# Performance work log

Measured on AMD Instinct MI355X. Metric: run time of the kernel, lower is better.

Reference implementation:

```python
import jax, jax.numpy as jnp
import numpy as np


def _conv2d(x, w, b):
    # x: [B,C,H,W], w: [O,I,kh,kw] (SAME padding, stride 1)
    y = jax.lax.conv_general_dilated(x, w, (1, 1), 'SAME',
                                     dimension_numbers=('NCHW', 'OIHW', 'NCHW'))
    return y + b[None, :, None, None]


def _conv1x1(x, w, b):
    # w: [O,C], b: [O]
    return jnp.einsum('oc,bchw->bohw', w, x) + b[None, :, None, None]


def _attention(xq, xkv, w, b):
    # w: [3,C,C] (q,k,v), b: [3,C]. Tokens = spatial positions, features = channels.
    B, C, H, W = xq.shape
    q = _conv1x1(xq, w[0], b[0]).reshape(B, C, H * W).transpose(0, 2, 1)   # [B,HW,C]
    k = _conv1x1(xkv, w[1], b[1]).reshape(B, C, H * W).transpose(0, 2, 1)
    v = _conv1x1(xkv, w[2], b[2]).reshape(B, C, H * W).transpose(0, 2, 1)
    scale = 1.0 / jnp.sqrt(jnp.asarray(C, xq.dtype))  # d_k = channels
    a = jax.nn.softmax(jnp.einsum('bnc,bmc->bnm', q, k) * scale, axis=-1)  # [B,HW,HW]
    out = jnp.einsum('bnm,bmc->bnc', a, v).transpose(0, 2, 1).reshape(B, C, H, W)
    return out + xq


def _cell(x, h, c, w, b):
    gates = _conv2d(jnp.concatenate([x, h], axis=1), w, b)
    i, f, o, g = jnp.split(gates, 4, axis=1)
    i, f, o, g = jax.nn.sigmoid(i), jax.nn.sigmoid(f), jax.nn.sigmoid(o), jnp.tanh(g)
    c_new = f * c + i * g
    h_new = o * jnp.tanh(c_new)
    return h_new, c_new


def setup_inputs() -> dict:
    key = jax.random.key(0)
    ks = iter(jax.random.split(key, 32))
    B, T, Cin, H, W = 2, 3, 1, 32, 32
    HID, L, K, OUT = 64, 2, 3, 1
    s = 0.02
    d = {
        'x1_seq': jax.random.normal(next(ks), (B, T, Cin, H, W), jnp.float32),
        'x2_seq': jax.random.normal(next(ks), (B, T, Cin, H, W), jnp.float32),
        # ConvLSTM gate convs: layer0 in = Cin+HID, layer1 in = 2*HID, per stream
        'conv1_w0': jax.random.normal(next(ks), (4 * HID, Cin + HID, K, K)) * s,
        'conv1_b0': jnp.zeros((4 * HID,)),
        'conv1_w1': jax.random.normal(next(ks), (4 * HID, 2 * HID, K, K)) * s,
        'conv1_b1': jnp.zeros((4 * HID,)),
        'conv2_w0': jax.random.normal(next(ks), (4 * HID, Cin + HID, K, K)) * s,
        'conv2_b0': jnp.zeros((4 * HID,)),
        'conv2_w1': jax.random.normal(next(ks), (4 * HID, 2 * HID, K, K)) * s,
        'conv2_b1': jnp.zeros((4 * HID,)),
        # attention 1x1 convs, stacked [L, 3(q/k/v), HID, HID]
        'sah_w': jax.random.normal(next(ks), (L, 3, HID, HID)) * s,
        'sah_b': jnp.zeros((L, 3, HID)),
        'sac_w': jax.random.normal(next(ks), (L, 3, HID, HID)) * s,
        'sac_b': jnp.zeros((L, 3, HID)),
        'cah_w': jax.random.normal(next(ks), (L, 3, HID, HID)) * s,
        'cah_b': jnp.zeros((L, 3, HID)),
        'cac_w': jax.random.normal(next(ks), (L, 3, HID, HID)) * s,
        'cac_b': jnp.zeros((L, 3, HID)),
        # decoder
        'dec_w1': jax.random.normal(next(ks), (HID, HID, 3, 3)) * s,
        'dec_b1': jnp.zeros((HID,)),
        'dec_w2': jax.random.normal(next(ks), (OUT, HID, 3, 3)) * s,
        'dec_b2': jnp.zeros((OUT,)),
        'future_steps': 4,
    }
    return d


def reference(x1_seq, x2_seq,
              conv1_w0, conv1_b0, conv1_w1, conv1_b1,
              conv2_w0, conv2_b0, conv2_w1, conv2_b1,
              sah_w, sah_b, sac_w, sac_b, cah_w, cah_b, cac_w, cac_b,
              dec_w1, dec_b1, dec_w2, dec_b2, future_steps):
    B, T, _, H, W = x1_seq.shape
    HID = sah_w.shape[-1]
    L = sah_w.shape[0]
    cw1 = [(conv1_w0, conv1_b0), (conv1_w1, conv1_b1)]
    cw2 = [(conv2_w0, conv2_b0), (conv2_w1, conv2_b1)]

    def decoder(h):
        return _conv2d(jax.nn.relu(_conv2d(h, dec_w1, dec_b1)), dec_w2, dec_b2)

    z = jnp.zeros((B, HID, H, W), x1_seq.dtype)
    h1s, c1s = [z] * L, [z] * L
    h2s, c2s = [z] * L, [z] * L

    def step(x1_t, x2_t, h1s, c1s, h2s, c2s):
        h1s, c1s, h2s, c2s = list(h1s), list(c1s), list(h2s), list(c2s)
        for l in range(L):
            h1, c1 = _cell(x1_t, h1s[l], c1s[l], *cw1[l])
            h2, c2 = _cell(x2_t, h2s[l], c2s[l], *cw2[l])
            h1 = _attention(h1, h1, sah_w[l], sah_b[l])
            c1 = _attention(c1, c1, sac_w[l], sac_b[l])
            h2 = _attention(h2, h2, sah_w[l], sah_b[l])
            c2 = _attention(c2, c2, sac_w[l], sac_b[l])
            tag_h1, tag_c1 = h1, c1
            h1 = _attention(h1, h2, cah_w[l], cah_b[l])
            c1 = _attention(c1, c2, cac_w[l], cac_b[l])
            h2 = _attention(h2, tag_h1, cah_w[l], cah_b[l])
            c2 = _attention(c2, tag_c1, cac_w[l], cac_b[l])
            h1s[l], c1s[l], h2s[l], c2s[l] = h1, c1, h2, c2
            x1_t, x2_t = h1, h2
        return h1s, c1s, h2s, c2s

    warm1, warm2 = [], []
    for t in range(T):
        h1s, c1s, h2s, c2s = step(x1_seq[:, t], x2_seq[:, t], h1s, c1s, h2s, c2s)
        if t < T - 1:
            warm1.append(h1s[-1])
            warm2.append(h2s[-1])
    pred_warm1 = jnp.stack([decoder(h) for h in warm1], axis=1)
    pred_warm2 = jnp.stack([decoder(h) for h in warm2], axis=1)

    preds1, preds2 = [], []
    for _ in range(int(future_steps)):
        p1 = decoder(h1s[-1])
        p2 = decoder(h2s[-1])
        preds1.append(p1)
        preds2.append(p2)
        h1s, c1s, h2s, c2s = step(p1, p2, h1s, c1s, h2s, c2s)
    preds1 = jnp.stack(preds1, axis=1)
    preds2 = jnp.stack(preds2, axis=1)
    return preds1, preds2, pred_warm1, pred_warm2
```

## Files before the change

### kernel.cpp

```cpp
#include <hip/hip_runtime.h>
#include <math.h>

#define BB 2
#define HIDC 64
#define HWN 1024

struct TWArgs { const float* src[5]; float* dst[5]; int icn9[5]; int osh[5]; };

__global__ __launch_bounds__(256) void transpose_w(TWArgs a) {
  const int arr = blockIdx.y;
  const int icn9 = a.icn9[arr], osh = a.osh[arr];
  const int ocn = 1 << osh;
  const float* s = a.src[arr];
  float* d = a.dst[arr];
  const int n = icn9 << osh;
  for (int i = blockIdx.x * 256 + threadIdx.x; i < n; i += gridDim.x * 256) {
    int oc = i & (ocn - 1), tt = i >> osh;
    d[i] = s[(size_t)oc * icn9 + tt];
  }
}

struct CellArgs {
  const float* x[2]; long xbs;
  const float* h[2]; const float* c[2];
  const float* w[2]; const float* bias[2];
  float* ho[2]; float* co[2];
};

template<int CX>
__global__ __launch_bounds__(512) void cell_kernel(CellArgs a) {
  constexpr int CT = CX + HIDC;
  constexpr int CH = (CT + 1) / 2;
  __shared__ float sIn[CT * 48];
  __shared__ float sGa[256 * 17];
  __shared__ float sGb[256 * 17];
  const int tile = blockIdx.x;
  const int b = blockIdx.y;
  const int st = blockIdx.z;
  const int ty0 = (tile >> 3) << 2, tx0 = (tile & 7) << 2;
  const float* xp = a.x[st] + (size_t)b * a.xbs;
  const float* hp = a.h[st] + (size_t)b * HIDC * HWN;

  for (int idx = threadIdx.x; idx < CT * 36; idx += 512) {
    int ic = idx / 36, pos = idx - ic * 36;
    int iy = pos / 6, ix = pos - iy * 6;
    int gy = ty0 - 1 + iy, gx = tx0 - 1 + ix;
    float v = 0.f;
    if ((unsigned)gy < 32u && (unsigned)gx < 32u) {
      v = (ic < CX) ? xp[ic * HWN + gy * 32 + gx]
                    : hp[(ic - CX) * HWN + gy * 32 + gx];
    }
    sIn[ic * 48 + iy * 8 + ix] = v;
  }
  __syncthreads();

  const int oc = threadIdx.x & 255;
  const int hh = threadIdx.x >> 8;
  const int icb = hh ? CH : 0, ice = hh ? CT : CH;
  float acc[16];
#pragma unroll
  for (int p = 0; p < 16; ++p) acc[p] = 0.f;
  const float* wp = a.w[st];
  for (int ic = icb; ic < ice; ++ic) {
    float w9[9];
#pragma unroll
    for (int t = 0; t < 9; ++t) w9[t] = wp[(ic * 9 + t) * 256 + oc];
    float in[36];
#pragma unroll
    for (int iy = 0; iy < 6; ++iy) {
      float4 v4 = *(const float4*)&sIn[ic * 48 + iy * 8];
      float2 v2 = *(const float2*)&sIn[ic * 48 + iy * 8 + 4];
      in[iy * 6 + 0] = v4.x; in[iy * 6 + 1] = v4.y; in[iy * 6 + 2] = v4.z;
      in[iy * 6 + 3] = v4.w; in[iy * 6 + 4] = v2.x; in[iy * 6 + 5] = v2.y;
    }
#pragma unroll
    for (int ky = 0; ky < 3; ++ky)
#pragma unroll
      for (int kx = 0; kx < 3; ++kx) {
        const float wv = w9[ky * 3 + kx];
#pragma unroll
        for (int py = 0; py < 4; ++py)
#pragma unroll
          for (int px = 0; px < 4; ++px)
            acc[py * 4 + px] += wv * in[(py + ky) * 6 + (px + kx)];
      }
  }
  float* sGh = hh ? sGb : sGa;
#pragma unroll
  for (int p = 0; p < 16; ++p) sGh[oc * 17 + p] = acc[p];
  __syncthreads();

  const float* cp = a.c[st] + (size_t)b * HIDC * HWN;
  float* hop = a.ho[st] + (size_t)b * HIDC * HWN;
  float* cop = a.co[st] + (size_t)b * HIDC * HWN;
  const float* bias = a.bias[st];
  for (int idx = threadIdx.x; idx < HIDC * 16; idx += 512) {
    int hc = idx >> 4, p = idx & 15;
    float gi = sGa[hc * 17 + p]         + sGb[hc * 17 + p]         + bias[hc];
    float gf = sGa[(hc + 64) * 17 + p]  + sGb[(hc + 64) * 17 + p]  + bias[hc + 64];
    float go = sGa[(hc + 128) * 17 + p] + sGb[(hc + 128) * 17 + p] + bias[hc + 128];
    float gg = sGa[(hc + 192) * 17 + p] + sGb[(hc + 192) * 17 + p] + bias[hc + 192];
    gi = 1.f / (1.f + expf(-gi));
    gf = 1.f / (1.f + expf(-gf));
    go = 1.f / (1.f + expf(-go));
    gg = tanhf(gg);
    int off = hc * HWN + (ty0 + (p >> 2)) * 32 + tx0 + (p & 3);
    float cn = gf * cp[off] + gi * gg;
    cop[off] = cn;
    hop[off] = go * tanhf(cn);
  }
}

struct QkvArgs {
  const float* xq[4]; const float* xkv[4];
  const float* w[4]; const float* bias[4];
  float* Q; float* K; float* V;
};

__global__ __launch_bounds__(256) void qkv_kernel(QkvArgs a) {
  __shared__ float sWt[64 * 68];
  const int ptile = blockIdx.x, b = blockIdx.y;
  const int attn = blockIdx.z / 3, proj = blockIdx.z % 3;
  const float* x = (proj == 0 ? a.xq[attn] : a.xkv[attn]) + (size_t)b * HIDC * HWN;
  const float* w = a.w[attn] + proj * 64 * 64;
  const float* bias = a.bias[attn] + proj * 64;
  const size_t bb = (size_t)attn * BB + b;
  for (int i = threadIdx.x; i < 4096; i += 256) {
    int o = i >> 6, c = i & 63;
    sWt[c * 68 + o] = w[i];
  }
  __syncthreads();
  const int pq = threadIdx.x & 63, og = threadIdx.x >> 6;
  const int p0 = ptile * 64 + pq;
  float acc[16];
#pragma unroll
  for (int k = 0; k < 16; ++k) acc[k] = bias[og * 16 + k];
  for (int c = 0; c < 64; ++c) {
    float xv = x[c * HWN + p0];
#pragma unroll
    for (int k = 0; k < 16; k += 4) {
      float4 wv = *(const float4*)&sWt[c * 68 + og * 16 + k];
      acc[k+0] += xv * wv.x; acc[k+1] += xv * wv.y;
      acc[k+2] += xv * wv.z; acc[k+3] += xv * wv.w;
    }
  }
  if (proj == 1) {
    float* dK = a.K + bb * HIDC * HWN;
#pragma unroll
    for (int k = 0; k < 16; ++k)
      dK[(size_t)(og * 16 + k) * HWN + p0] = acc[k];
  } else {
    float* dst = (proj == 0 ? a.Q : a.V) + bb * HWN * HIDC;
    float* d = dst + (size_t)p0 * HIDC + og * 16;
#pragma unroll
    for (int k = 0; k < 16; k += 4) {
      float4 v; v.x = acc[k]; v.y = acc[k+1]; v.z = acc[k+2]; v.w = acc[k+3];
      *(float4*)&d[k] = v;
    }
  }
}

struct AttnPArgs { const float* Q; const float* Kt; const float* V; float* pbuf; };

__global__ __launch_bounds__(256) void attn_part(AttnPArgs a) {
  __shared__ float sQt[64 * 64];
  __shared__ float sPt[64 * 64];
  const int qt = blockIdx.x >> 3, ks = blockIdx.x & 7;
  const int b = blockIdx.y, at = blockIdx.z;
  const size_t bb = (size_t)at * BB + b;
  const float* Qp  = a.Q  + bb * HWN * HIDC + (size_t)qt * 64 * HIDC;
  const float* Ktp = a.Kt + bb * HIDC * HWN;
  const float* Vp  = a.V  + bb * HWN * HIDC;
  const int tid = threadIdx.x;
  {
    const int qr = tid & 63, qc0 = (tid >> 6) * 16;
    const float* q = Qp + qr * HIDC + qc0;
#pragma unroll
    for (int k = 0; k < 16; k += 4) {
      float4 v = *(const float4*)&q[k];
      sQt[(qc0 + k + 0) * 64 + qr] = v.x * 0.125f;
      sQt[(qc0 + k + 1) * 64 + qr] = v.y * 0.125f;
      sQt[(qc0 + k + 2) * 64 + qr] = v.z * 0.125f;
      sQt[(qc0 + k + 3) * 64 + qr] = v.w * 0.125f;
    }
  }
  const int tc = tid & 15, tr = tid >> 4;
  const int j0 = tc * 4, r0 = tr * 4;
  float m[4], l[4], o[4][4];
#pragma unroll
  for (int i = 0; i < 4; ++i) {
    m[i] = -1e30f; l[i] = 0.f;
    o[i][0] = 0; o[i][1] = 0; o[i][2] = 0; o[i][3] = 0;
  }
  __syncthreads();

  for (int kk = 0; kk < 2; ++kk) {
    const int jg = (ks * 2 + kk) * 64;
    float s[4][4];
#pragma unroll
    for (int i = 0; i < 4; ++i) { s[i][0]=0; s[i][1]=0; s[i][2]=0; s[i][3]=0; }
    const float* kp = Ktp + jg + j0;
#pragma unroll 8
    for (int c = 0; c < 64; ++c) {
      float4 q4 = *(const float4*)&sQt[c * 64 + r0];
      float4 k4 = *(const float4*)&kp[(size_t)c * HWN];
      s[0][0]+=q4.x*k4.x; s[0][1]+=q4.x*k4.y; s[0][2]+=q4.x*k4.z; s[0][3]+=q4.x*k4.w;
      s[1][0]+=q4.y*k4.x; s[1][1]+=q4.y*k4.y; s[1][2]+=q4.y*k4.z; s[1][3]+=q4.y*k4.w;
      s[2][0]+=q4.z*k4.x; s[2][1]+=q4.z*k4.y; s[2][2]+=q4.z*k4.z; s[2][3]+=q4.z*k4.w;
      s[3][0]+=q4.w*k4.x; s[3][1]+=q4.w*k4.y; s[3][2]+=q4.w*k4.z; s[3][3]+=q4.w*k4.w;
    }
    float mt[4];
#pragma unroll
    for (int i = 0; i < 4; ++i)
      mt[i] = fmaxf(fmaxf(s[i][0], s[i][1]), fmaxf(s[i][2], s[i][3]));
#pragma unroll
    for (int d = 1; d < 16; d <<= 1) {
#pragma unroll
      for (int i = 0; i < 4; ++i) mt[i] = fmaxf(mt[i], __shfl_xor(mt[i], d));
    }
    float al[4];
#pragma unroll
    for (int i = 0; i < 4; ++i) {
      float mn = fmaxf(m[i], mt[i]);
      al[i] = __expf(m[i] - mn);
      m[i] = mn;
      s[i][0] = __expf(s[i][0] - mn); s[i][1] = __expf(s[i][1] - mn);
      s[i][2] = __expf(s[i][2] - mn); s[i][3] = __expf(s[i][3] - mn);
    }
    float ps[4];
#pragma unroll
    for (int i = 0; i < 4; ++i) ps[i] = s[i][0] + s[i][1] + s[i][2] + s[i][3];
#pragma unroll
    for (int d = 1; d < 16; d <<= 1) {
#pragma unroll
      for (int i = 0; i < 4; ++i) ps[i] += __shfl_xor(ps[i], d);
    }
#pragma unroll
    for (int i = 0; i < 4; ++i) {
      l[i] = l[i] * al[i] + ps[i];
      o[i][0] *= al[i]; o[i][1] *= al[i]; o[i][2] *= al[i]; o[i][3] *= al[i];
    }
    __syncthreads();
#pragma unroll
    for (int jj = 0; jj < 4; ++jj) {
      int j = j0 + jj;
      float4 pv; pv.x = s[0][jj]; pv.y = s[1][jj]; pv.z = s[2][jj]; pv.w = s[3][jj];
      *(float4*)&sPt[j * 64 + (r0 ^ ((j & 7) * 4))] = pv;
    }
    __syncthreads();
    const float* vp = Vp + (size_t)jg * HIDC + j0;
#pragma unroll 8
    for (int j = 0; j < 64; ++j) {
      float4 p4 = *(const float4*)&sPt[j * 64 + (r0 ^ ((j & 7) * 4))];
      float4 v4 = *(const float4*)&vp[(size_t)j * HIDC];
      o[0][0]+=p4.x*v4.x; o[0][1]+=p4.x*v4.y; o[0][2]+=p4.x*v4.z; o[0][3]+=p4.x*v4.w;
      o[1][0]+=p4.y*v4.x; o[1][1]+=p4.y*v4.y; o[1][2]+=p4.y*v4.z; o[1][3]+=p4.y*v4.w;
      o[2][0]+=p4.z*v4.x; o[2][1]+=p4.z*v4.y; o[2][2]+=p4.z*v4.z; o[2][3]+=p4.z*v4.w;
      o[3][0]+=p4.w*v4.x; o[3][1]+=p4.w*v4.y; o[3][2]+=p4.w*v4.z; o[3][3]+=p4.w*v4.w;
    }
  }
  float* pb = a.pbuf + ((bb * 16 + qt) * 8 + ks) * 4224;
#pragma unroll
  for (int i = 0; i < 4; ++i) {
    float4 w; w.x = o[i][0]; w.y = o[i][1]; w.z = o[i][2]; w.w = o[i][3];
    *(float4*)&pb[(r0 + i) * 64 + j0] = w;
  }
  if (tc == 0) {
#pragma unroll
    for (int i = 0; i < 4; ++i) {
      pb[4096 + r0 + i] = m[i];
      pb[4160 + r0 + i] = l[i];
    }
  }
}

struct AttnMArgs { const float* pbuf; const float* xq[4]; float* out[4]; };

__global__ __launch_bounds__(256) void attn_merge(AttnMArgs a) {
  __shared__ float sW[8][64];
  __shared__ float sL[64];
  const int qt = blockIdx.x, b = blockIdx.y, at = blockIdx.z;
  const float* pb = a.pbuf + (((size_t)at * BB + b) * 16 + qt) * 8 * 4224;
  if (threadIdx.x < 64) {
    int r = threadIdx.x;
    float mm[8];
#pragma unroll
    for (int i = 0; i < 8; ++i) mm[i] = pb[i * 4224 + 4096 + r];
    float M = mm[0];
#pragma unroll
    for (int i = 1; i < 8; ++i) M = fmaxf(M, mm[i]);
    float L = 0.f;
#pragma unroll
    for (int i = 0; i < 8; ++i) {
      float w = __expf(mm[i] - M);
      sW[i][r] = w;
      L += pb[i * 4224 + 4160 + r] * w;
    }
    sL[r] = L;
  }
  __syncthreads();
  const int c = threadIdx.x >> 2, rg = (threadIdx.x & 3) * 16;
  const float* xq = a.xq[at] + (size_t)b * HIDC * HWN;
  float* op = a.out[at] + (size_t)b * HIDC * HWN;
  const int p0 = qt * 64 + rg;
#pragma unroll
  for (int rr4 = 0; rr4 < 16; rr4 += 4) {
    float rv[4];
#pragma unroll
    for (int k = 0; k < 4; ++k) {
      int r = rg + rr4 + k;
      float acc = 0.f;
#pragma unroll
      for (int i = 0; i < 8; ++i) acc += pb[i * 4224 + r * 64 + c] * sW[i][r];
      rv[k] = acc / sL[r];
    }
    float4 x4 = *(const float4*)&xq[(size_t)c * HWN + p0 + rr4];
    float4 res; res.x = rv[0] + x4.x; res.y = rv[1] + x4.y;
    res.z = rv[2] + x4.z; res.w = rv[3] + x4.w;
    *(float4*)&op[(size_t)c * HWN + p0 + rr4] = res;
  }
}

struct Dec1Args { const float* in[2]; const float* w; const float* b; float* tmp; };

__global__ __launch_bounds__(512) void dec1_kernel(Dec1Args a) {
  __shared__ float sIn[64 * 48];
  __shared__ float sHa[64 * 17];
  __shared__ float sHb[64 * 17];
  const int tile = blockIdx.x, b = blockIdx.y, st = blockIdx.z;
  const int ty0 = (tile >> 3) << 2, tx0 = (tile & 7) << 2;
  const float* ip = a.in[st] + (size_t)b * HIDC * HWN;
  for (int idx = threadIdx.x; idx < 64 * 36; idx += 512) {
    int ic = idx / 36, pos = idx - ic * 36;
    int iy = pos / 6, ix = pos - iy * 6;
    int gy = ty0 - 1 + iy, gx = tx0 - 1 + ix;
    float v = 0.f;
    if ((unsigned)gy < 32u && (unsigned)gx < 32u) v = ip[ic * HWN + gy * 32 + gx];
    sIn[ic * 48 + iy * 8 + ix] = v;
  }
  __syncthreads();
  const int oc = threadIdx.x & 63, ps = (threadIdx.x >> 6) & 3;
  const int hh = threadIdx.x >> 8;
  const int icb = hh * 32, ice = icb + 32;
  float acc0 = 0.f, acc1 = 0.f, acc2 = 0.f, acc3 = 0.f;
  const float* wp = a.w;
  for (int ic = icb; ic < ice; ++ic) {
    float w9[9];
#pragma unroll
    for (int t = 0; t < 9; ++t) w9[t] = wp[(ic * 9 + t) * 64 + oc];
    float in[18];
#pragma unroll
    for (int ry = 0; ry < 3; ++ry) {
      float4 v4 = *(const float4*)&sIn[ic * 48 + (ps + ry) * 8];
      float2 v2 = *(const float2*)&sIn[ic * 48 + (ps + ry) * 8 + 4];
      in[ry*6+0]=v4.x; in[ry*6+1]=v4.y; in[ry*6+2]=v4.z; in[ry*6+3]=v4.w;
      in[ry*6+4]=v2.x; in[ry*6+5]=v2.y;
    }
#pragma unroll
    for (int ky = 0; ky < 3; ++ky)
#pragma unroll
      for (int kx = 0; kx < 3; ++kx) {
        float wv = w9[ky * 3 + kx];
        acc0 += wv * in[ky * 6 + kx + 0];
        acc1 += wv * in[ky * 6 + kx + 1];
        acc2 += wv * in[ky * 6 + kx + 2];
        acc3 += wv * in[ky * 6 + kx + 3];
      }
  }
  float* sH = hh ? sHb : sHa;
  sH[oc * 17 + ps * 4 + 0] = acc0;
  sH[oc * 17 + ps * 4 + 1] = acc1;
  sH[oc * 17 + ps * 4 + 2] = acc2;
  sH[oc * 17 + ps * 4 + 3] = acc3;
  __syncthreads();
  float* dst = a.tmp + ((size_t)st * BB + b) * HIDC * HWN;
  for (int idx = threadIdx.x; idx < 1024; idx += 512) {
    int oc2 = idx >> 4, p = idx & 15;
    float v = sHa[oc2 * 17 + p] + sHb[oc2 * 17 + p] + a.b[oc2];
    v = fmaxf(v, 0.f);
    dst[(size_t)oc2 * HWN + (ty0 + (p >> 2)) * 32 + tx0 + (p & 3)] = v;
  }
}

struct Dec2Args { const float* tmp; const float* w; const float* b;
                  float* dst0; float* dst1; long bstr; };

__global__ __launch_bounds__(256) void dec2_kernel(Dec2Args a) {
  __shared__ float sIn[64 * 48];
  __shared__ float sW[64 * 9];
  const int tile = blockIdx.x, b = blockIdx.y, st = blockIdx.z;
  const int ty0 = (tile >> 3) << 2, tx0 = (tile & 7) << 2;
  const float* ip = a.tmp + ((size_t)st * BB + b) * HIDC * HWN;
  for (int idx = threadIdx.x; idx < 64 * 36; idx += 256) {
    int ic = idx / 36, pos = idx - ic * 36;
    int iy = pos / 6, ix = pos - iy * 6;
    int gy = ty0 - 1 + iy, gx = tx0 - 1 + ix;
    float v = 0.f;
    if ((unsigned)gy < 32u && (unsigned)gx < 32u) v = ip[ic * HWN + gy * 32 + gx];
    sIn[ic * 48 + iy * 8 + ix] = v;
  }
  for (int idx = threadIdx.x; idx < 576; idx += 256) sW[idx] = a.w[idx];
  __syncthreads();
  const int px = threadIdx.x >> 4, icg = threadIdx.x & 15;
  const int py = px >> 2, pxx = px & 3;
  float acc = 0.f;
#pragma unroll
  for (int i = 0; i < 4; ++i) {
    int ic = icg * 4 + i;
    const float* row = &sIn[ic * 48];
    const float* wv = &sW[ic * 9];
#pragma unroll
    for (int ky = 0; ky < 3; ++ky)
#pragma unroll
      for (int kx = 0; kx < 3; ++kx)
        acc += wv[ky * 3 + kx] * row[(py + ky) * 8 + pxx + kx];
  }
#pragma unroll
  for (int d = 1; d < 16; d <<= 1) acc += __shfl_xor(acc, d);
  if (icg == 0) {
    float* d = (st == 0 ? a.dst0 : a.dst1);
    d[(size_t)b * a.bstr + (ty0 + py) * 32 + tx0 + pxx] = acc + a.b[0];
  }
}

extern "C" void kernel_launch(void* const* d_in, const int* in_sizes, int n_in,
                              void* d_out, int out_size, void* d_ws, size_t ws_size,
                              hipStream_t stream) {
  (void)in_sizes; (void)n_in; (void)out_size; (void)ws_size;
  const float* x1_seq = (const float*)d_in[0];
  const float* x2_seq = (const float*)d_in[1];
  const float* c1w[2] = {(const float*)d_in[2], (const float*)d_in[4]};
  const float* c1b[2] = {(const float*)d_in[3], (const float*)d_in[5]};
  const float* c2w[2] = {(const float*)d_in[6], (const float*)d_in[8]};
  const float* c2b[2] = {(const float*)d_in[7], (const float*)d_in[9]};
  const float* sah_w = (const float*)d_in[10]; const float* sah_b = (const float*)d_in[11];
  const float* sac_w = (const float*)d_in[12]; const float* sac_b = (const float*)d_in[13];
  const float* cah_w = (const float*)d_in[14]; const float* cah_b = (const float*)d_in[15];
  const float* cac_w = (const float*)d_in[16]; const float* cac_b = (const float*)d_in[17];
  const float* dw1 = (const float*)d_in[18]; const float* db1 = (const float*)d_in[19];
  const float* dw2 = (const float*)d_in[20]; const float* db2 = (const float*)d_in[21];
  float* out = (float*)d_out;
  float* ws = (float*)d_ws;

  const size_t SPL = (size_t)BB * HIDC * HWN;
  float* h1s = ws;
  float* c1s = h1s + 2 * SPL;
  float* h2s = c1s + 2 * SPL;
  float* c2s = h2s + 2 * SPL;
  float* hc1 = c2s + 2 * SPL;
  float* cc1 = hc1 + SPL;
  float* hc2 = cc1 + SPL;
  float* cc2 = hc2 + SPL;
  float* hs1 = cc2 + SPL;
  float* cs1 = hs1 + SPL;
  float* hs2 = cs1 + SPL;
  float* cs2 = hs2 + SPL;
  float* Qb  = cs2 + SPL;
  float* Kb  = Qb + 4 * SPL;
  float* Vb  = Kb + 4 * SPL;
  float* dtmp = Vb + 4 * SPL;
  float* pbuf = dtmp + 2 * SPL;
  float* wt10 = pbuf + (size_t)4 * BB * 16 * 8 * 4224;
  float* wt11 = wt10 + 585 * 256;
  float* wt20 = wt11 + 1152 * 256;
  float* wt21 = wt20 + 585 * 256;
  float* wtd  = wt21 + 1152 * 256;

  hipMemsetAsync(ws, 0, 8 * SPL * sizeof(float), stream);

  const dim3 blk(256);
  const dim3 blk2(512);

  {
    TWArgs tw;
    tw.src[0] = c1w[0]; tw.dst[0] = wt10; tw.icn9[0] = 585;  tw.osh[0] = 8;
    tw.src[1] = c1w[1]; tw.dst[1] = wt11; tw.icn9[1] = 1152; tw.osh[1] = 8;
    tw.src[2] = c2w[0]; tw.dst[2] = wt20; tw.icn9[2] = 585;  tw.osh[2] = 8;
    tw.src[3] = c2w[1]; tw.dst[3] = wt21; tw.icn9[3] = 1152; tw.osh[3] = 8;
    tw.src[4] = dw1;    tw.dst[4] = wtd;  tw.icn9[4] = 576;  tw.osh[4] = 6;
    transpose_w<<<dim3(32, 5), blk, 0, stream>>>(tw);
  }

  auto attn_stage = [&](const float* q0, const float* q1, const float* q2, const float* q3,
                        const float* k0, const float* k1, const float* k2, const float* k3,
                        const float* wh, const float* bh, const float* wc, const float* bc,
                        float* o0, float* o1, float* o2, float* o3) {
    QkvArgs qa;
    qa.xq[0]=q0; qa.xq[1]=q1; qa.xq[2]=q2; qa.xq[3]=q3;
    qa.xkv[0]=k0; qa.xkv[1]=k1; qa.xkv[2]=k2; qa.xkv[3]=k3;
    qa.w[0]=wh; qa.w[1]=wc; qa.w[2]=wh; qa.w[3]=wc;
    qa.bias[0]=bh; qa.bias[1]=bc; qa.bias[2]=bh; qa.bias[3]=bc;
    qa.Q=Qb; qa.K=Kb; qa.V=Vb;
    qkv_kernel<<<dim3(16, BB, 12), blk, 0, stream>>>(qa);
    AttnPArgs ap; ap.Q=Qb; ap.Kt=Kb; ap.V=Vb; ap.pbuf=pbuf;
    attn_part<<<dim3(128, BB, 4), blk, 0, stream>>>(ap);
    AttnMArgs am; am.pbuf=pbuf;
    am.xq[0]=q0; am.xq[1]=q1; am.xq[2]=q2; am.xq[3]=q3;
    am.out[0]=o0; am.out[1]=o1; am.out[2]=o2; am.out[3]=o3;
    attn_merge<<<dim3(16, BB, 4), blk, 0, stream>>>(am);
  };

  auto decode = [&](long off1, long off2, long bstr) {
    Dec1Args d1; d1.in[0] = h1s + SPL; d1.in[1] = h2s + SPL;
    d1.w = wtd; d1.b = db1; d1.tmp = dtmp;
    dec1_kernel<<<dim3(64, BB, 2), blk2, 0, stream>>>(d1);
    Dec2Args d2; d2.tmp = dtmp; d2.w = dw2; d2.b = db2;
    d2.dst0 = out + off1; d2.dst1 = out + off2; d2.bstr = bstr;
    dec2_kernel<<<dim3(64, BB, 2), blk, 0, stream>>>(d2);
  };

  for (int s = 0; s < 6; ++s) {
    const float *x1, *x2; long xbs;
    if (s < 3) { x1 = x1_seq + s * HWN; x2 = x2_seq + s * HWN; xbs = 3 * HWN; }
    else       { x1 = out + (s - 3) * HWN; x2 = out + 8192 + (s - 3) * HWN; xbs = 4 * HWN; }

    for (int l = 0; l < 2; ++l) {
      if (l == 1) { x1 = h1s; x2 = h2s; xbs = (long)HIDC * HWN; }
      CellArgs ca;
      ca.x[0] = x1; ca.x[1] = x2; ca.xbs = xbs;
      ca.h[0] = h1s + l * SPL; ca.h[1] = h2s + l * SPL;
      ca.c[0] = c1s + l * SPL; ca.c[1] = c2s + l * SPL;
      ca.w[0] = (l == 0) ? wt10 : wt11;
      ca.w[1] = (l == 0) ? wt20 : wt21;
      ca.bias[0] = c1b[l]; ca.bias[1] = c2b[l];
      ca.ho[0] = hc1; ca.ho[1] = hc2; ca.co[0] = cc1; ca.co[1] = cc2;
      if (l == 0) cell_kernel<1><<<dim3(64, BB, 2), blk2, 0, stream>>>(ca);
      else        cell_kernel<64><<<dim3(64, BB, 2), blk2, 0, stream>>>(ca);

      attn_stage(hc1, cc1, hc2, cc2,
                 hc1, cc1, hc2, cc2,
                 sah_w + l * 12288, sah_b + l * 192,
                 sac_w + l * 12288, sac_b + l * 192,
                 hs1, cs1, hs2, cs2);
      attn_stage(hs1, cs1, hs2, cs2,
                 hs2, cs2, hs1, cs1,
                 cah_w + l * 12288, cah_b + l * 192,
                 cac_w + l * 12288, cac_b + l * 192,
                 h1s + l * SPL, c1s + l * SPL, h2s + l * SPL, c2s + l * SPL);
    }

    if (s == 0)      decode(16384,        20480,        2048);
    else if (s == 1) decode(16384 + 1024, 20480 + 1024, 2048);
    else             decode((s - 2) * HWN, 8192 + (s - 2) * HWN, 4096);
  }
}
```

Measured before the change: 2.527 ms.

## Compute attention with fp16 MFMA using hi/lo split for fp32-level accuracy

The QKV projection now writes Q, K and V as pairs of fp16 high and low parts, with the softmax scale folded into Q and V stored transposed. The attention kernel replaces scalar fp32 FMA loops with 16x16x32 fp16 MFMA instructions, using three products per pair (hi*hi, hi*lo, lo*hi) to approximate fp32 precision, and it does the same for the P*V product through a swizzled LDS tile. Key splitting drops from 8 to 4 partitions per query tile, which halves the partial buffer and the merge work. The cost is six times the MFMA issue per tile, extra conversion work, and some loss of precision compared with full fp32.

Result: faster. 2.073 ms (-18.0%).

```diff
diff --git a/kernel.cpp b/kernel.cpp
--- a/kernel.cpp
+++ b/kernel.cpp
@@ -4,6 +4,18 @@
 #define BB 2
 #define HIDC 64
 #define HWN 1024
+
+typedef _Float16 half8 __attribute__((ext_vector_type(8)));
+typedef float f32x4 __attribute__((ext_vector_type(4)));
+
+static __device__ __forceinline__ unsigned short f2h_bits(float v) {
+  _Float16 h = (_Float16)v;
+  return __builtin_bit_cast(unsigned short, h);
+}
+static __device__ __forceinline__ float h_back(float v) {
+  _Float16 h = (_Float16)v;
+  return (float)h;
+}
 
 struct TWArgs { const float* src[5]; float* dst[5]; int icn9[5]; int osh[5]; };
 
@@ -114,7 +126,7 @@
 struct QkvArgs {
   const float* xq[4]; const float* xkv[4];
   const float* w[4]; const float* bias[4];
-  float* Q; float* K; float* V;
+  unsigned short *Qh, *Ql, *Kh, *Kl, *Vth, *Vtl;
 };
 
 __global__ __launch_bounds__(256) void qkv_kernel(QkvArgs a) {
@@ -144,157 +156,174 @@
       acc[k+2] += xv * wv.z; acc[k+3] += xv * wv.w;
     }
   }
-  if (proj == 1) {
-    float* dK = a.K + bb * HIDC * HWN;
-#pragma unroll
-    for (int k = 0; k < 16; ++k)
-      dK[(size_t)(og * 16 + k) * HWN + p0] = acc[k];
+  if (proj <= 1) {
+    const float sc = (proj == 0) ? 0.125f : 1.f;
+    unsigned short* dh = (proj == 0 ? a.Qh : a.Kh) + (bb << 16) + p0 * 64 + og * 16;
+    unsigned short* dl = (proj == 0 ? a.Ql : a.Kl) + (bb << 16) + p0 * 64 + og * 16;
+#pragma unroll
+    for (int k = 0; k < 16; k += 2) {
+      float v0 = acc[k] * sc, v1 = acc[k+1] * sc;
+      unsigned short h0 = f2h_bits(v0), h1 = f2h_bits(v1);
+      *(unsigned int*)&dh[k] = (unsigned int)h0 | ((unsigned int)h1 << 16);
+      unsigned short l0 = f2h_bits(v0 - h_back(v0)), l1 = f2h_bits(v1 - h_back(v1));
+      *(unsigned int*)&dl[k] = (unsigned int)l0 | ((unsigned int)l1 << 16);
+    }
   } else {
-    float* dst = (proj == 0 ? a.Q : a.V) + bb * HWN * HIDC;
-    float* d = dst + (size_t)p0 * HIDC + og * 16;
-#pragma unroll
-    for (int k = 0; k < 16; k += 4) {
-      float4 v; v.x = acc[k]; v.y = acc[k+1]; v.z = acc[k+2]; v.w = acc[k+3];
-      *(float4*)&d[k] = v;
-    }
-  }
-}
-
-struct AttnPArgs { const float* Q; const float* Kt; const float* V; float* pbuf; };
+    unsigned short* dvh = a.Vth + (bb << 16);
+    unsigned short* dvl = a.Vtl + (bb << 16);
+#pragma unroll
+    for (int k = 0; k < 16; ++k) {
+      float v = acc[k];
+      dvh[(size_t)(og * 16 + k) * HWN + p0] = f2h_bits(v);
+      dvl[(size_t)(og * 16 + k) * HWN + p0] = f2h_bits(v - h_back(v));
+    }
+  }
+}
+
+struct AttnPArgs {
+  const unsigned short *Qh, *Ql, *Kh, *Kl, *Vth, *Vtl;
+  float* pbuf;
+};
 
 __global__ __launch_bounds__(256) void attn_part(AttnPArgs a) {
-  __shared__ float sQt[64 * 64];
-  __shared__ float sPt[64 * 64];
-  const int qt = blockIdx.x >> 3, ks = blockIdx.x & 7;
+  __shared__ unsigned short sP[4][2][16][72];
+  const int qt = blockIdx.x >> 2, ks = blockIdx.x & 3;
   const int b = blockIdx.y, at = blockIdx.z;
   const size_t bb = (size_t)at * BB + b;
-  const float* Qp  = a.Q  + bb * HWN * HIDC + (size_t)qt * 64 * HIDC;
-  const float* Ktp = a.Kt + bb * HIDC * HWN;
-  const float* Vp  = a.V  + bb * HWN * HIDC;
   const int tid = threadIdx.x;
-  {
-    const int qr = tid & 63, qc0 = (tid >> 6) * 16;
-    const float* q = Qp + qr * HIDC + qc0;
-#pragma unroll
-    for (int k = 0; k < 16; k += 4) {
-      float4 v = *(const float4*)&q[k];
-      sQt[(qc0 + k + 0) * 64 + qr] = v.x * 0.125f;
-      sQt[(qc0 + k + 1) * 64 + qr] = v.y * 0.125f;
-      sQt[(qc0 + k + 2) * 64 + qr] = v.z * 0.125f;
-      sQt[(qc0 + k + 3) * 64 + qr] = v.w * 0.125f;
-    }
-  }
-  const int tc = tid & 15, tr = tid >> 4;
-  const int j0 = tc * 4, r0 = tr * 4;
-  float m[4], l[4], o[4][4];
-#pragma unroll
-  for (int i = 0; i < 4; ++i) {
-    m[i] = -1e30f; l[i] = 0.f;
-    o[i][0] = 0; o[i][1] = 0; o[i][2] = 0; o[i][3] = 0;
-  }
-  __syncthreads();
-
-  for (int kk = 0; kk < 2; ++kk) {
-    const int jg = (ks * 2 + kk) * 64;
-    float s[4][4];
-#pragma unroll
-    for (int i = 0; i < 4; ++i) { s[i][0]=0; s[i][1]=0; s[i][2]=0; s[i][3]=0; }
-    const float* kp = Ktp + jg + j0;
-#pragma unroll 8
-    for (int c = 0; c < 64; ++c) {
-      float4 q4 = *(const float4*)&sQt[c * 64 + r0];
-      float4 k4 = *(const float4*)&kp[(size_t)c * HWN];
-      s[0][0]+=q4.x*k4.x; s[0][1]+=q4.x*k4.y; s[0][2]+=q4.x*k4.z; s[0][3]+=q4.x*k4.w;
-      s[1][0]+=q4.y*k4.x; s[1][1]+=q4.y*k4.y; s[1][2]+=q4.y*k4.z; s[1][3]+=q4.y*k4.w;
-      s[2][0]+=q4.z*k4.x; s[2][1]+=q4.z*k4.y; s[2][2]+=q4.z*k4.z; s[2][3]+=q4.z*k4.w;
-      s[3][0]+=q4.w*k4.x; s[3][1]+=q4.w*k4.y; s[3][2]+=q4.w*k4.z; s[3][3]+=q4.w*k4.w;
-    }
-    float mt[4];
-#pragma unroll
-    for (int i = 0; i < 4; ++i)
-      mt[i] = fmaxf(fmaxf(s[i][0], s[i][1]), fmaxf(s[i][2], s[i][3]));
-#pragma unroll
-    for (int d = 1; d < 16; d <<= 1) {
-#pragma unroll
-      for (int i = 0; i < 4; ++i) mt[i] = fmaxf(mt[i], __shfl_xor(mt[i], d));
-    }
-    float al[4];
+  const int w = tid >> 6, lane = tid & 63;
+  const int g = lane >> 4, qc = lane & 15;
+  const int swz = (qc & 7) << 3;
+  const unsigned short* Qhp = a.Qh + (bb << 16);
+  const unsigned short* Qlp = a.Ql + (bb << 16);
+  const unsigned short* Khp = a.Kh + (bb << 16);
+  const unsigned short* Klp = a.Kl + (bb << 16);
+  const unsigned short* Vhp = a.Vth + (bb << 16);
+  const unsigned short* Vlp = a.Vtl + (bb << 16);
+
+  const int qrow = qt * 64 + w * 16 + qc;
+  const half8 bqh0 = *(const half8*)&Qhp[qrow * 64 + 0  + g * 8];
+  const half8 bqh1 = *(const half8*)&Qhp[qrow * 64 + 32 + g * 8];
+  const half8 bql0 = *(const half8*)&Qlp[qrow * 64 + 0  + g * 8];
+  const half8 bql1 = *(const half8*)&Qlp[qrow * 64 + 32 + g * 8];
+
+  float mrun = -1e30f, lrun = 0.f;
+  f32x4 sO[4];
+#pragma unroll
+  for (int i = 0; i < 4; ++i) sO[i] = (f32x4)0.f;
+
+  for (int kk = 0; kk < 4; ++kk) {
+    const int jt = (ks * 4 + kk) * 64;
+    f32x4 sS[4];
+#pragma unroll
+    for (int i = 0; i < 4; ++i) sS[i] = (f32x4)0.f;
+#pragma unroll
+    for (int sb = 0; sb < 4; ++sb) {
+      const int j = jt + sb * 16 + qc;
+      const half8 ah0 = *(const half8*)&Khp[j * 64 + 0  + g * 8];
+      const half8 ah1 = *(const half8*)&Khp[j * 64 + 32 + g * 8];
+      const half8 al0 = *(const half8*)&Klp[j * 64 + 0  + g * 8];
+      const half8 al1 = *(const half8*)&Klp[j * 64 + 32 + g * 8];
+      f32x4 d = sS[sb];
+      d = __builtin_amdgcn_mfma_f32_16x16x32_f16(ah0, bqh0, d, 0, 0, 0);
+      d = __builtin_amdgcn_mfma_f32_16x16x32_f16(ah1, bqh1, d, 0, 0, 0);
+      d = __builtin_amdgcn_mfma_f32_16x16x32_f16(ah0, bql0, d, 0, 0, 0);
+      d = __builtin_amdgcn_mfma_f32_16x16x32_f16(ah1, bql1, d, 0, 0, 0);
+      d = __builtin_amdgcn_mfma_f32_16x16x32_f16(al0, bqh0, d, 0, 0, 0);
+      d = __builtin_amdgcn_mfma_f32_16x16x32_f16(al1, bqh1, d, 0, 0, 0);
+      sS[sb] = d;
+    }
+    float mt = -1e30f;
+#pragma unroll
+    for (int sb = 0; sb < 4; ++sb)
+#pragma unroll
+      for (int r = 0; r < 4; ++r) mt = fmaxf(mt, sS[sb][r]);
+    mt = fmaxf(mt, __shfl_xor(mt, 16));
+    mt = fmaxf(mt, __shfl_xor(mt, 32));
+    const float mn = fmaxf(mrun, mt);
+    const float al = __expf(mrun - mn);
+    float p[16];
+    float ps = 0.f;
+#pragma unroll
+    for (int sb = 0; sb < 4; ++sb)
+#pragma unroll
+      for (int r = 0; r < 4; ++r) {
+        float e = __expf(sS[sb][r] - mn);
+        p[sb * 4 + r] = e; ps += e;
+      }
+    ps += __shfl_xor(ps, 16);
+    ps += __shfl_xor(ps, 32);
+    lrun = lrun * al + ps;
+    mrun = mn;
 #pragma unroll
     for (int i = 0; i < 4; ++i) {
-      float mn = fmaxf(m[i], mt[i]);
-      al[i] = __expf(m[i] - mn);
-      m[i] = mn;
-      s[i][0] = __expf(s[i][0] - mn); s[i][1] = __expf(s[i][1] - mn);
-      s[i][2] = __expf(s[i][2] - mn); s[i][3] = __expf(s[i][3] - mn);
-    }
-    float ps[4];
-#pragma unroll
-    for (int i = 0; i < 4; ++i) ps[i] = s[i][0] + s[i][1] + s[i][2] + s[i][3];
-#pragma unroll
-    for (int d = 1; d < 16; d <<= 1) {
-#pragma unroll
-      for (int i = 0; i < 4; ++i) ps[i] += __shfl_xor(ps[i], d);
-    }
-#pragma unroll
-    for (int i = 0; i < 4; ++i) {
-      l[i] = l[i] * al[i] + ps[i];
-      o[i][0] *= al[i]; o[i][1] *= al[i]; o[i][2] *= al[i]; o[i][3] *= al[i];
-    }
-    __syncthreads();
-#pragma unroll
-    for (int jj = 0; jj < 4; ++jj) {
-      int j = j0 + jj;
-      float4 pv; pv.x = s[0][jj]; pv.y = s[1][jj]; pv.z = s[2][jj]; pv.w = s[3][jj];
-      *(float4*)&sPt[j * 64 + (r0 ^ ((j & 7) * 4))] = pv;
-    }
-    __syncthreads();
-    const float* vp = Vp + (size_t)jg * HIDC + j0;
-#pragma unroll 8
-    for (int j = 0; j < 64; ++j) {
-      float4 p4 = *(const float4*)&sPt[j * 64 + (r0 ^ ((j & 7) * 4))];
-      float4 v4 = *(const float4*)&vp[(size_t)j * HIDC];
-      o[0][0]+=p4.x*v4.x; o[0][1]+=p4.x*v4.y; o[0][2]+=p4.x*v4.z; o[0][3]+=p4.x*v4.w;
-      o[1][0]+=p4.y*v4.x; o[1][1]+=p4.y*v4.y; o[1][2]+=p4.y*v4.z; o[1][3]+=p4.y*v4.w;
-      o[2][0]+=p4.z*v4.x; o[2][1]+=p4.z*v4.y; o[2][2]+=p4.z*v4.z; o[2][3]+=p4.z*v4.w;
-      o[3][0]+=p4.w*v4.x; o[3][1]+=p4.w*v4.y; o[3][2]+=p4.w*v4.z; o[3][3]+=p4.w*v4.w;
-    }
-  }
-  float* pb = a.pbuf + ((bb * 16 + qt) * 8 + ks) * 4224;
-#pragma unroll
-  for (int i = 0; i < 4; ++i) {
-    float4 w; w.x = o[i][0]; w.y = o[i][1]; w.z = o[i][2]; w.w = o[i][3];
-    *(float4*)&pb[(r0 + i) * 64 + j0] = w;
-  }
-  if (tc == 0) {
-#pragma unroll
-    for (int i = 0; i < 4; ++i) {
-      pb[4096 + r0 + i] = m[i];
-      pb[4160 + r0 + i] = l[i];
-    }
+      sO[i][0] *= al; sO[i][1] *= al; sO[i][2] *= al; sO[i][3] *= al;
+    }
+#pragma unroll
+    for (int sb = 0; sb < 4; ++sb)
+#pragma unroll
+      for (int rp = 0; rp < 4; rp += 2) {
+        int j = sb * 16 + g * 4 + rp;
+        int js = j ^ swz;
+        float v0 = p[sb * 4 + rp], v1 = p[sb * 4 + rp + 1];
+        unsigned short h0 = f2h_bits(v0), h1 = f2h_bits(v1);
+        *(unsigned int*)&sP[w][0][qc][js] = (unsigned int)h0 | ((unsigned int)h1 << 16);
+        unsigned short l0 = f2h_bits(v0 - h_back(v0)), l1 = f2h_bits(v1 - h_back(v1));
+        *(unsigned int*)&sP[w][1][qc][js] = (unsigned int)l0 | ((unsigned int)l1 << 16);
+      }
+    const half8 ph0 = *(const half8*)&sP[w][0][qc][((0 + g) ^ (qc & 7)) * 8];
+    const half8 ph1 = *(const half8*)&sP[w][0][qc][((4 + g) ^ (qc & 7)) * 8];
+    const half8 pl0 = *(const half8*)&sP[w][1][qc][((0 + g) ^ (qc & 7)) * 8];
+    const half8 pl1 = *(const half8*)&sP[w][1][qc][((4 + g) ^ (qc & 7)) * 8];
+#pragma unroll
+    for (int vs = 0; vs < 4; ++vs) {
+      const int vc = vs * 16 + qc;
+      const half8 vh0 = *(const half8*)&Vhp[(size_t)vc * HWN + jt + 0  + g * 8];
+      const half8 vh1 = *(const half8*)&Vhp[(size_t)vc * HWN + jt + 32 + g * 8];
+      const half8 vl0 = *(const half8*)&Vlp[(size_t)vc * HWN + jt + 0  + g * 8];
+      const half8 vl1 = *(const half8*)&Vlp[(size_t)vc * HWN + jt + 32 + g * 8];
+      f32x4 d = sO[vs];
+      d = __builtin_amdgcn_mfma_f32_16x16x32_f16(vh0, ph0, d, 0, 0, 0);
+      d = __builtin_amdgcn_mfma_f32_16x16x32_f16(vh1, ph1, d, 0, 0, 0);
+      d = __builtin_amdgcn_mfma_f32_16x16x32_f16(vh0, pl0, d, 0, 0, 0);
+      d = __builtin_amdgcn_mfma_f32_16x16x32_f16(vh1, pl1, d, 0, 0, 0);
+      d = __builtin_amdgcn_mfma_f32_16x16x32_f16(vl0, ph0, d, 0, 0, 0);
+      d = __builtin_amdgcn_mfma_f32_16x16x32_f16(vl1, ph1, d, 0, 0, 0);
+      sO[vs] = d;
+    }
+  }
+  float* pb = a.pbuf + ((bb * 16 + qt) * 4 + ks) * 4224;
+  const int qloc = w * 16 + qc;
+#pragma unroll
+  for (int vs = 0; vs < 4; ++vs)
+#pragma unroll
+    for (int r = 0; r < 4; ++r)
+      pb[qloc * 64 + vs * 16 + g * 4 + r] = sO[vs][r];
+  if (g == 0) {
+    pb[4096 + qloc] = mrun;
+    pb[4160 + qloc] = lrun;
   }
 }
 
 struct AttnMArgs { const float* pbuf; const float* xq[4]; float* out[4]; };
 
 __global__ __launch_bounds__(256) void attn_merge(AttnMArgs a) {
-  __shared__ float sW[8][64];
+  __shared__ float sW[4][64];
   __shared__ float sL[64];
   const int qt = blockIdx.x, b = blockIdx.y, at = blockIdx.z;
-  const float* pb = a.pbuf + (((size_t)at * BB + b) * 16 + qt) * 8 * 4224;
+  const float* pb = a.pbuf + (((size_t)at * BB + b) * 16 + qt) * 4 * 4224;
   if (threadIdx.x < 64) {
     int r = threadIdx.x;
-    float mm[8];
-#pragma unroll
-    for (int i = 0; i < 8; ++i) mm[i] = pb[i * 4224 + 4096 + r];
-    float M = mm[0];
-#pragma unroll
-    for (int i = 1; i < 8; ++i) M = fmaxf(M, mm[i]);
+    float mm[4];
+#pragma unroll
+    for (int i = 0; i < 4; ++i) mm[i] = pb[i * 4224 + 4096 + r];
+    float M = fmaxf(fmaxf(mm[0], mm[1]), fmaxf(mm[2], mm[3]));
     float L = 0.f;
 #pragma unroll
-    for (int i = 0; i < 8; ++i) {
-      float w = __expf(mm[i] - M);
-      sW[i][r] = w;
-      L += pb[i * 4224 + 4160 + r] * w;
+    for (int i = 0; i < 4; ++i) {
+      float wv = __expf(mm[i] - M);
+      sW[i][r] = wv;
+      L += pb[i * 4224 + 4160 + r] * wv;
     }
     sL[r] = L;
   }
@@ -311,7 +340,7 @@
       int r = rg + rr4 + k;
       float acc = 0.f;
 #pragma unroll
-      for (int i = 0; i < 8; ++i) acc += pb[i * 4224 + r * 64 + c] * sW[i][r];
+      for (int i = 0; i < 4; ++i) acc += pb[i * 4224 + r * 64 + c] * sW[i][r];
       rv[k] = acc / sL[r];
     }
     float4 x4 = *(const float4*)&xq[(size_t)c * HWN + p0 + rr4];
@@ -455,12 +484,15 @@
   float* cs1 = hs1 + SPL;
   float* hs2 = cs1 + SPL;
   float* cs2 = hs2 + SPL;
-  float* Qb  = cs2 + SPL;
-  float* Kb  = Qb + 4 * SPL;
-  float* Vb  = Kb + 4 * SPL;
-  float* dtmp = Vb + 4 * SPL;
+  float* Qf  = cs2 + SPL;
+  float* Kf  = Qf + 4 * SPL;
+  float* Vf  = Kf + 4 * SPL;
+  unsigned short* Qh = (unsigned short*)Qf;  unsigned short* Ql = Qh + (size_t)8 * 65536;
+  unsigned short* Kh = (unsigned short*)Kf;  unsigned short* Kl = Kh + (size_t)8 * 65536;
+  unsigned short* Vth = (unsigned short*)Vf; unsigned short* Vtl = Vth + (size_t)8 * 65536;
+  float* dtmp = Vf + 4 * SPL;
   float* pbuf = dtmp + 2 * SPL;
-  float* wt10 = pbuf + (size_t)4 * BB * 16 * 8 * 4224;
+  float* wt10 = pbuf + (size_t)4 * BB * 16 * 4 * 4224;
   float* wt11 = wt10 + 585 * 256;
   float* wt20 = wt11 + 1152 * 256;
   float* wt21 = wt20 + 585 * 256;
@@ -490,10 +522,11 @@
     qa.xkv[0]=k0; qa.xkv[1]=k1; qa.xkv[2]=k2; qa.xkv[3]=k3;
     qa.w[0]=wh; qa.w[1]=wc; qa.w[2]=wh; qa.w[3]=wc;
     qa.bias[0]=bh; qa.bias[1]=bc; qa.bias[2]=bh; qa.bias[3]=bc;
-    qa.Q=Qb; qa.K=Kb; qa.V=Vb;
+    qa.Qh=Qh; qa.Ql=Ql; qa.Kh=Kh; qa.Kl=Kl; qa.Vth=Vth; qa.Vtl=Vtl;
     qkv_kernel<<<dim3(16, BB, 12), blk, 0, stream>>>(qa);
-    AttnPArgs ap; ap.Q=Qb; ap.Kt=Kb; ap.V=Vb; ap.pbuf=pbuf;
-    attn_part<<<dim3(128, BB, 4), blk, 0, stream>>>(ap);
+    AttnPArgs ap; ap.Qh=Qh; ap.Ql=Ql; ap.Kh=Kh; ap.Kl=Kl; ap.Vth=Vth; ap.Vtl=Vtl;
+    ap.pbuf=pbuf;
+    attn_part<<<dim3(64, BB, 4), blk, 0, stream>>>(ap);
     AttnMArgs am; am.pbuf=pbuf;
     am.xq[0]=q0; am.xq[1]=q1; am.xq[2]=q2; am.xq[3]=q3;
     am.out[0]=o0; am.out[1]=o1; am.out[2]=o2; am.out[3]=o3;
```
